# Kernel optimization log

Measured on AMD Instinct MI355X. Metric: run time of the kernel, lower is better.

## Reference

```python
import jax, jax.numpy as jnp
import numpy as np

N, E = 10000, 80000
D, D_EDGE, L = 32, 16, 3
D2 = D * D


def layer_norm(x, g, b, eps=1e-5):
    m = jnp.mean(x, axis=-1, keepdims=True)
    v = jnp.var(x, axis=-1, keepdims=True)
    return (x - m) / jnp.sqrt(v + eps) * g + b


def setup_inputs() -> dict:
    key = jax.random.key(0)
    ks = jax.random.split(key, 16)
    s_e = 1.0 / np.sqrt(D_EDGE)
    s_d = 1.0 / np.sqrt(D)
    s_f = 1.0 / np.sqrt(L * D)
    return {
        "x": jax.random.normal(ks[0], (N, D), dtype=jnp.float32),
        "edge_index": jax.random.randint(ks[1], (2, E), 0, N),
        "edge_attr": jax.random.normal(ks[2], (E, D_EDGE), dtype=jnp.float32),
        # shared edge MLP: Linear(d_edge_in -> d^2) + LayerNorm(d^2) + ReLU
        "emlp_w": jax.random.uniform(ks[3], (D2, D_EDGE), jnp.float32, -s_e, s_e),
        "emlp_b": jnp.zeros((D2,), jnp.float32),
        "emlp_ln_g": jnp.ones((D2,), jnp.float32),
        "emlp_ln_b": jnp.zeros((D2,), jnp.float32),
        # per-layer params (stacked over L layers)
        "root_w": jax.random.uniform(ks[4], (L, D, D), jnp.float32, -s_d, s_d),  # NNConv root lin (no bias)
        "conv_b": jnp.zeros((L, D), jnp.float32),                                # NNConv bias
        "res_w": jax.random.uniform(ks[5], (L, D, D), jnp.float32, -s_d, s_d),
        "res_b": jnp.zeros((L, D), jnp.float32),
        "ln_g": jnp.ones((L, D), jnp.float32),
        "ln_b": jnp.zeros((L, D), jnp.float32),
        # fusion: Linear(L*d -> d) + LayerNorm(d) + ReLU
        "fuse_w": jax.random.uniform(ks[6], (D, L * D), jnp.float32, -s_f, s_f),
        "fuse_b": jnp.zeros((D,), jnp.float32),
        "fuse_ln_g": jnp.ones((D,), jnp.float32),
        "fuse_ln_b": jnp.zeros((D,), jnp.float32),
    }


def reference(x, edge_index, edge_attr, emlp_w, emlp_b, emlp_ln_g, emlp_ln_b,
              root_w, conv_b, res_w, res_b, ln_g, ln_b,
              fuse_w, fuse_b, fuse_ln_g, fuse_ln_b):
    n_nodes = x.shape[0]
    src, tgt = edge_index[0], edge_index[1]
    # Shared edge MLP applied to the same edge_attr in every layer -> identical
    # per-edge weight matrices; compute once. [E, d_in, d_out]
    h = layer_norm(edge_attr @ emlp_w.T + emlp_b, emlp_ln_g, emlp_ln_b)
    We = jax.nn.relu(h).reshape(-1, D, D)
    x_src_gatherer = src
    outputs = []
    for l in range(L):
        x_res = x @ res_w[l].T + res_b[l]
        # NNConv message: x_j @ W_e, scatter-add to target nodes
        msg = jnp.einsum('ed,edf->ef', x[x_src_gatherer], We)  # [E, d]
        agg = jax.ops.segment_sum(msg, tgt, num_segments=n_nodes)
        h = agg + x @ root_w[l].T + conv_b[l]
        # dropout is identity in eval mode
        x = layer_norm(h + x_res, ln_g[l], ln_b[l])
        outputs.append(x)
    fused = jnp.concatenate(outputs, axis=-1) @ fuse_w.T + fuse_b
    fused = jax.nn.relu(layer_norm(fused, fuse_ln_g, fuse_ln_b))
    return fused
```

## Files before the change

kernel.cpp:

```cpp
#include <hip/hip_runtime.h>

#define NN 10000
#define EE 80000
#define DD 32
#define DEDGE 16
#define LL 3
#define D2V 1024
#define NTILE 2500

typedef __attribute__((ext_vector_type(8))) short short8v;
typedef __attribute__((ext_vector_type(16))) float f32x16;

__device__ __forceinline__ unsigned short bf16rne(float x) {
    unsigned u = __float_as_uint(x);
    return (unsigned short)((u + 0x7FFF + ((u >> 16) & 1)) >> 16);
}
__device__ __forceinline__ float bf16tof(unsigned short h) {
    return __uint_as_float(((unsigned)h) << 16);
}
__device__ __forceinline__ uint4 pack8(const unsigned short* u) {
    uint4 r;
    r.x = (unsigned)u[0] | ((unsigned)u[1] << 16);
    r.y = (unsigned)u[2] | ((unsigned)u[3] << 16);
    r.z = (unsigned)u[4] | ((unsigned)u[5] << 16);
    r.w = (unsigned)u[6] | ((unsigned)u[7] << 16);
    return r;
}

__global__ __launch_bounds__(256) void setup1_kernel(
    const int* __restrict__ ei,
    const float* __restrict__ w, const float* __restrict__ wb,
    const float* __restrict__ lg, const float* __restrict__ lb,
    int* __restrict__ cnt, float* __restrict__ st,
    uint4* __restrict__ afh, uint4* __restrict__ afl, uint4* __restrict__ a2f) {
    const int bid = blockIdx.x;
    const int t = threadIdx.x;
    if (bid < 313) {
        const int e = bid * 256 + t;
        if (e < EE) atomicAdd(&cnt[ei[EE + e]], 1);
    } else if (bid < 377) {
        const int r0 = (bid - 313) * 16;
        const int k = t >> 4, j = t & 15;
        float acc = 0.f;
#pragma unroll
        for (int r = 0; r < 16; ++r)
            acc = fmaf(w[(r0 + r) * DEDGE + k], w[(r0 + r) * DEDGE + j], acc);
        atomicAdd(&st[t], acc * (1.f / D2V));
        if (t < DEDGE) {
            float s = 0.f, q = 0.f;
#pragma unroll
            for (int r = 0; r < 16; ++r) {
                s += w[(r0 + r) * DEDGE + t];
                q = fmaf(wb[r0 + r], w[(r0 + r) * DEDGE + t], q);
            }
            atomicAdd(&st[256 + t], s * (1.f / D2V));
            atomicAdd(&st[272 + t], q * (1.f / D2V));
        } else if (t == 16) {
            float s = 0.f, s2 = 0.f;
#pragma unroll
            for (int r = 0; r < 16; ++r) {
                s += wb[r0 + r];
                s2 = fmaf(wb[r0 + r], wb[r0 + r], s2);
            }
            atomicAdd(&st[288], s * (1.f / D2V));
            atomicAdd(&st[289], s2 * (1.f / D2V));
        }
    } else {
        const int tid = (bid - 377) * 256 + t;
        if (tid >= 32 * 64) return;
        const int d = tid >> 6, l = tid & 63;
        const int row = l & 31, kh = l >> 5;
        const int r = d * 32 + row;
        const float g = lg[r];
        unsigned short uh[8], ul[8];
#pragma unroll
        for (int i = 0; i < 8; ++i) {
            const float v = g * w[r * DEDGE + kh * 8 + i];
            const unsigned short h = bf16rne(v);
            uh[i] = h;
            ul[i] = bf16rne(v - bf16tof(h));
        }
        afh[d * 64 + l] = pack8(uh);
        afl[d * 64 + l] = pack8(ul);
        if (kh == 0) {
            const float bg = g * wb[r];
            const float lbv = lb[r];
            const unsigned short bgh = bf16rne(bg);
            const unsigned short bgl = bf16rne(bg - bf16tof(bgh));
            const unsigned short gh = bf16rne(g);
            const unsigned short gl = bf16rne(g - bf16tof(gh));
            const unsigned short lbh = bf16rne(lbv);
            const unsigned short lbl = bf16rne(lbv - bf16tof(lbh));
            unsigned short sarr[8] = {bgh, bgl, bgh, gh, gl, gh, lbh, lbl};
            a2f[d * 64 + l] = pack8(sarr);
        } else {
            a2f[d * 64 + l] = make_uint4(0, 0, 0, 0);
        }
    }
}

__global__ __launch_bounds__(1024) void scan_kernel(int* __restrict__ cur, int* __restrict__ off) {
    __shared__ int s[1024];
    const int t = threadIdx.x;
    const int base = t * 10;
    int loc[10];
    int run = 0;
#pragma unroll
    for (int i = 0; i < 10; ++i) {
        const int idx = base + i;
        const int v = (idx < NN) ? cur[idx] : 0;
        loc[i] = run;
        run += v;
    }
    s[t] = run;
    __syncthreads();
    for (int o = 1; o < 1024; o <<= 1) {
        const int v = (t >= o) ? s[t - o] : 0;
        __syncthreads();
        s[t] += v;
        __syncthreads();
    }
    const int excl = s[t] - run;
#pragma unroll
    for (int i = 0; i < 10; ++i) {
        const int idx = base + i;
        if (idx < NN) {
            off[idx] = excl + loc[i];
            cur[idx] = excl + loc[i];
        }
    }
    if (t == 1023) off[NN] = s[1023];
}

__global__ __launch_bounds__(256) void stats_edge_perm2(const float* __restrict__ eattr,
                                                        const float* __restrict__ st,
                                                        const int* __restrict__ ei,
                                                        int* __restrict__ cur,
                                                        uint4* __restrict__ bfh,
                                                        uint4* __restrict__ bfl,
                                                        uint4* __restrict__ b2f,
                                                        int* __restrict__ sperm) {
    const int e = blockIdx.x * 256 + threadIdx.x;
    if (e >= EE) return;
    const int tgt = ei[EE + e];
    const int p = atomicAdd(&cur[tgt], 1);
    sperm[p] = ei[e];
    float ea[16];
    {
        const float4* ep = (const float4*)(eattr + e * DEDGE);
#pragma unroll
        for (int c = 0; c < 4; ++c) {
            const float4 t4 = ep[c];
            ea[4 * c] = t4.x; ea[4 * c + 1] = t4.y; ea[4 * c + 2] = t4.z; ea[4 * c + 3] = t4.w;
        }
    }
    float m = st[288];
#pragma unroll
    for (int k = 0; k < 16; ++k) m = fmaf(st[256 + k], ea[k], m);
    float ex2 = st[289];
#pragma unroll
    for (int k = 0; k < 16; ++k) {
        float tv = 2.f * st[272 + k];
#pragma unroll
        for (int j = 0; j < 16; ++j) tv = fmaf(st[k * 16 + j], ea[j], tv);
        ex2 = fmaf(tv, ea[k], ex2);
    }
    const float var = fmaxf(ex2 - m * m, 0.f);
    const float inv = rsqrtf(var + 1e-5f);
    const float nmi = -m * inv;
    const int tt = p >> 5, col = p & 31;
#pragma unroll
    for (int h = 0; h < 2; ++h) {
        unsigned short uh[8], ul[8];
#pragma unroll
        for (int i = 0; i < 8; ++i) {
            const float v = inv * ea[8 * h + i];
            const unsigned short a = bf16rne(v);
            uh[i] = a;
            ul[i] = bf16rne(v - bf16tof(a));
        }
        bfh[tt * 64 + h * 32 + col] = pack8(uh);
        bfl[tt * 64 + h * 32 + col] = pack8(ul);
    }
    const unsigned short ivh = bf16rne(inv);
    const unsigned short ivl = bf16rne(inv - bf16tof(ivh));
    const unsigned short nmh = bf16rne(nmi);
    const unsigned short nml = bf16rne(nmi - bf16tof(nmh));
    const unsigned short one = 0x3F80;
    unsigned short s[8] = {ivh, ivh, ivl, nmh, nmh, nml, one, one};
    b2f[tt * 64 + col] = pack8(s);
    b2f[tt * 64 + 32 + col] = make_uint4(0, 0, 0, 0);
}

__global__ __launch_bounds__(512) void edge_mfma_lds(
    const float* __restrict__ x, const int* __restrict__ sperm,
    const uint4* __restrict__ afh, const uint4* __restrict__ afl, const uint4* __restrict__ a2f,
    const uint4* __restrict__ bfh, const uint4* __restrict__ bfl, const uint4* __restrict__ b2f,
    float* __restrict__ msgout) {
    __shared__ uint4 lafh[2048];
    __shared__ uint4 lafl[2048];
    __shared__ uint4 la2c[1024];
    const int t = threadIdx.x;
    for (int i = t; i < 2048; i += 512) {
        lafh[i] = afh[i];
        lafl[i] = afl[i];
    }
    for (int i = t; i < 1024; i += 512)
        la2c[i] = a2f[(i >> 5) * 64 + (i & 31)];
    __syncthreads();

    const int lane = t & 63;
    const int w = blockIdx.x * 8 + (t >> 6);
    if (w >= NTILE) return;
    const int col = lane & 31, hi = lane >> 5;
    const int p = w * 32 + col;
    const int si = sperm[p];
    float xr[32];
    {
        const float4* xp = (const float4*)(x + si * DD);
#pragma unroll
        for (int c = 0; c < 8; ++c) {
            const float4 t4 = xp[c];
            xr[4 * c] = t4.x; xr[4 * c + 1] = t4.y; xr[4 * c + 2] = t4.z; xr[4 * c + 3] = t4.w;
        }
    }
    const short8v bh = ((const short8v*)bfh)[w * 64 + lane];
    const short8v bl = ((const short8v*)bfl)[w * 64 + lane];
    const short8v b2 = ((const short8v*)b2f)[w * 64 + lane];
    float mg[16];
#pragma unroll
    for (int i = 0; i < 16; ++i) mg[i] = 0.f;
#pragma unroll
    for (int d = 0; d < 32; ++d) {
        const short8v ah = ((const short8v*)lafh)[d * 64 + lane];
        const short8v al = ((const short8v*)lafl)[d * 64 + lane];
        const short8v a2 = ((const short8v*)la2c)[d * 32 + col];
        f32x16 C;
#pragma unroll
        for (int r = 0; r < 16; ++r) C[r] = 0.f;
        C = __builtin_amdgcn_mfma_f32_32x32x16_bf16(ah, bh, C, 0, 0, 0);
        C = __builtin_amdgcn_mfma_f32_32x32x16_bf16(ah, bl, C, 0, 0, 0);
        C = __builtin_amdgcn_mfma_f32_32x32x16_bf16(al, bh, C, 0, 0, 0);
        C = __builtin_amdgcn_mfma_f32_32x32x16_bf16(a2, b2, C, 0, 0, 0);
        const float xd = xr[d];
#pragma unroll
        for (int r = 0; r < 16; ++r) mg[r] = fmaf(xd, fmaxf(C[r], 0.f), mg[r]);
    }
    float* op = msgout + p * DD + hi * 4;
#pragma unroll
    for (int q = 0; q < 4; ++q)
        *(float4*)(op + q * 8) = make_float4(mg[4 * q], mg[4 * q + 1], mg[4 * q + 2], mg[4 * q + 3]);
}

__global__ __launch_bounds__(256) void node_wave_kernel(
    const float* __restrict__ x, const float* __restrict__ msg,
    const int* __restrict__ off,
    const float* __restrict__ root_w, const float* __restrict__ conv_b,
    const float* __restrict__ res_w, const float* __restrict__ res_b,
    const float* __restrict__ lng, const float* __restrict__ lnb,
    float* __restrict__ out) {
    const int lane = threadIdx.x & 63;
    const int w = (blockIdx.x * 256 + threadIdx.x) >> 6;
    const int hi = lane >> 5, f = lane & 31;
    const int n = w * 2 + hi;
    float wrow[32];
    {
        const float4* rp = (const float4*)(root_w + f * DD);
        const float4* sp = (const float4*)(res_w + f * DD);
#pragma unroll
        for (int c = 0; c < 8; ++c) {
            const float4 a = rp[c];
            const float4 b = sp[c];
            wrow[4 * c] = a.x + b.x; wrow[4 * c + 1] = a.y + b.y;
            wrow[4 * c + 2] = a.z + b.z; wrow[4 * c + 3] = a.w + b.w;
        }
    }
    float acc = conv_b[f] + res_b[f];
    const int k0 = off[n], k1 = off[n + 1];
    for (int k = k0; k < k1; ++k) acc += msg[k * DD + f];
    const float xl = x[n * DD + f];
#pragma unroll
    for (int d = 0; d < DD; ++d) acc = fmaf(__shfl(xl, hi * 32 + d), wrow[d], acc);
    float s1 = acc, s2 = acc * acc;
#pragma unroll
    for (int o = 16; o >= 1; o >>= 1) {
        s1 += __shfl_xor(s1, o);
        s2 += __shfl_xor(s2, o);
    }
    const float m = s1 * (1.f / 32.f);
    const float v = s2 * (1.f / 32.f) - m * m;
    const float inv = rsqrtf(v + 1e-5f);
    out[n * DD + f] = fmaf((acc - m) * inv, lng[f], lnb[f]);
}

__global__ __launch_bounds__(256) void node_fuse_kernel(
    const float* __restrict__ x, const float* __restrict__ msg,
    const int* __restrict__ off,
    const float* __restrict__ root_w, const float* __restrict__ conv_b,
    const float* __restrict__ res_w, const float* __restrict__ res_b,
    const float* __restrict__ lng, const float* __restrict__ lnb,
    const float* __restrict__ o0, const float* __restrict__ o1,
    const float* __restrict__ fw, const float* __restrict__ fb,
    const float* __restrict__ fg, const float* __restrict__ fbb,
    float* __restrict__ out) {
    const int lane = threadIdx.x & 63;
    const int w = (blockIdx.x * 256 + threadIdx.x) >> 6;
    const int hi = lane >> 5, f = lane & 31;
    const int n = w * 2 + hi;
    float o2v;
    {
        float wrow[32];
        {
            const float4* rp = (const float4*)(root_w + f * DD);
            const float4* sp = (const float4*)(res_w + f * DD);
#pragma unroll
            for (int c = 0; c < 8; ++c) {
                const float4 a = rp[c];
                const float4 b = sp[c];
                wrow[4 * c] = a.x + b.x; wrow[4 * c + 1] = a.y + b.y;
                wrow[4 * c + 2] = a.z + b.z; wrow[4 * c + 3] = a.w + b.w;
            }
        }
        float acc = conv_b[f] + res_b[f];
        const int k0 = off[n], k1 = off[n + 1];
        for (int k = k0; k < k1; ++k) acc += msg[k * DD + f];
        const float xl = x[n * DD + f];
#pragma unroll
        for (int d = 0; d < DD; ++d) acc = fmaf(__shfl(xl, hi * 32 + d), wrow[d], acc);
        float s1 = acc, s2 = acc * acc;
#pragma unroll
        for (int o = 16; o >= 1; o >>= 1) {
            s1 += __shfl_xor(s1, o);
            s2 += __shfl_xor(s2, o);
        }
        const float m = s1 * (1.f / 32.f);
        const float v = s2 * (1.f / 32.f) - m * m;
        const float inv = rsqrtf(v + 1e-5f);
        o2v = fmaf((acc - m) * inv, lng[f], lnb[f]);
    }
    float fr[96];
    {
        const float4* fp = (const float4*)(fw + f * 96);
#pragma unroll
        for (int c = 0; c < 24; ++c) {
            const float4 t4 = fp[c];
            fr[4 * c] = t4.x; fr[4 * c + 1] = t4.y; fr[4 * c + 2] = t4.z; fr[4 * c + 3] = t4.w;
        }
    }
    float acc = fb[f];
    const float c0 = o0[n * DD + f], c1 = o1[n * DD + f];
#pragma unroll
    for (int d = 0; d < DD; ++d) acc = fmaf(__shfl(c0, hi * 32 + d), fr[d], acc);
#pragma unroll
    for (int d = 0; d < DD; ++d) acc = fmaf(__shfl(c1, hi * 32 + d), fr[32 + d], acc);
#pragma unroll
    for (int d = 0; d < DD; ++d) acc = fmaf(__shfl(o2v, hi * 32 + d), fr[64 + d], acc);
    float s1 = acc, s2 = acc * acc;
#pragma unroll
    for (int o = 16; o >= 1; o >>= 1) {
        s1 += __shfl_xor(s1, o);
        s2 += __shfl_xor(s2, o);
    }
    const float m = s1 * (1.f / 32.f);
    const float v = s2 * (1.f / 32.f) - m * m;
    const float inv = rsqrtf(v + 1e-5f);
    out[n * DD + f] = fmaxf(fmaf((acc - m) * inv, fg[f], fbb[f]), 0.f);
}

extern "C" void kernel_launch(void* const* d_in, const int* in_sizes, int n_in,
                              void* d_out, int out_size, void* d_ws, size_t ws_size,
                              hipStream_t stream) {
    const float* x   = (const float*)d_in[0];
    const int*   ei  = (const int*)d_in[1];
    const float* ea  = (const float*)d_in[2];
    const float* emw = (const float*)d_in[3];
    const float* emb = (const float*)d_in[4];
    const float* elg = (const float*)d_in[5];
    const float* elb = (const float*)d_in[6];
    const float* rootw = (const float*)d_in[7];
    const float* convb = (const float*)d_in[8];
    const float* resw  = (const float*)d_in[9];
    const float* resb  = (const float*)d_in[10];
    const float* lng   = (const float*)d_in[11];
    const float* lnb   = (const float*)d_in[12];
    const float* fw    = (const float*)d_in[13];
    const float* fb    = (const float*)d_in[14];
    const float* flg   = (const float*)d_in[15];
    const float* flb   = (const float*)d_in[16];
    float* doutp = (float*)d_out;

    const size_t U4N = 2048 * 3 + (size_t)NTILE * 64 * 3;
    const size_t FR0 = U4N * 4;
    const size_t FTOT = FR0 + (size_t)EE * DD + 2 * (size_t)NN * DD + 320;
    const size_t ITOT = 2 * (NN + 1) + 2 * (size_t)EE;
    const size_t PRIMARY_NEED = FTOT * 4 + ITOT * 4 + 256;

    if (ws_size < PRIMARY_NEED) return;

    uint4* u4 = (uint4*)d_ws;
    uint4* afh = u4;
    uint4* afl = afh + 2048;
    uint4* a2f = afl + 2048;
    uint4* bfh = a2f + 2048;
    uint4* bfl = bfh + (size_t)NTILE * 64;
    uint4* b2f = bfl + (size_t)NTILE * 64;
    float* wsf = (float*)d_ws;
    float* msg  = wsf + FR0;
    float* out0 = msg + (size_t)EE * DD;
    float* out1 = out0 + NN * DD;
    float* st   = out1 + NN * DD;
    int* cur   = (int*)(st + 320);
    int* off   = cur + (NN + 1);
    int* spare = off + (NN + 1);
    int* sperm = spare + EE;
    (void)spare;

    hipMemsetAsync(st, 0, (320 + NN + 1) * sizeof(float), stream);
    setup1_kernel<<<385, 256, 0, stream>>>(ei, emw, emb, elg, elb, cur, st, afh, afl, a2f);
    scan_kernel<<<1, 1024, 0, stream>>>(cur, off);
    stats_edge_perm2<<<313, 256, 0, stream>>>(ea, st, ei, cur, bfh, bfl, b2f, sperm);

    edge_mfma_lds<<<313, 512, 0, stream>>>(x, sperm, afh, afl, a2f, bfh, bfl, b2f, msg);
    node_wave_kernel<<<1250, 256, 0, stream>>>(x, msg, off,
        rootw, convb, resw, resb, lng, lnb, out0);
    edge_mfma_lds<<<313, 512, 0, stream>>>(out0, sperm, afh, afl, a2f, bfh, bfl, b2f, msg);
    node_wave_kernel<<<1250, 256, 0, stream>>>(out0, msg, off,
        rootw + D2V, convb + DD, resw + D2V, resb + DD, lng + DD, lnb + DD, out1);
    edge_mfma_lds<<<313, 512, 0, stream>>>(out1, sperm, afh, afl, a2f, bfh, bfl, b2f, msg);
    node_fuse_kernel<<<1250, 256, 0, stream>>>(out1, msg, off,
        rootw + 2 * D2V, convb + 2 * DD, resw + 2 * D2V, resb + 2 * DD,
        lng + 2 * DD, lnb + 2 * DD,
        out0, out1, fw, fb, flg, flb, doutp);
}
```

Baseline: 169.8 us.

## Merge setup, scan and edge-permutation kernels into one grid-synchronized kernel

Replaces the setup kernel, the single-block scan kernel and the edge permutation/stats kernel with one persistent 385-block kernel that uses global atomic counters and spin-waits as grid barriers. Zeroing of the counters and stats now happens inside the kernel, so the large memset shrinks to a 4-int reset. The aim is to remove three launch gaps and the memset. In exchange it relies on all 385 blocks being co-resident, and the scan now runs in a single 256-thread block while the other blocks spin.

Result: slower. 304.5 us (+79.3%).

```diff
diff --git a/kernel.cpp b/kernel.cpp
--- a/kernel.cpp
+++ b/kernel.cpp
@@ -27,31 +27,52 @@
     return r;
 }
 
-__global__ __launch_bounds__(256) void setup1_kernel(
-    const int* __restrict__ ei,
-    const float* __restrict__ w, const float* __restrict__ wb,
-    const float* __restrict__ lg, const float* __restrict__ lb,
-    int* __restrict__ cnt, float* __restrict__ st,
-    uint4* __restrict__ afh, uint4* __restrict__ afl, uint4* __restrict__ a2f) {
+__device__ __forceinline__ void block_spin(int* p, int target) {
+    if (threadIdx.x == 0) {
+        while (atomicAdd(p, 0) < target) __builtin_amdgcn_s_sleep(16);
+    }
+    __syncthreads();
+    __threadfence();
+}
+
+__global__ __launch_bounds__(256) void merged_csr(
+    const int* __restrict__ ei, const float* __restrict__ eattr,
+    const float* __restrict__ emw, const float* __restrict__ emb,
+    const float* __restrict__ elg, const float* __restrict__ elb,
+    int* __restrict__ syncc, int* __restrict__ cur, int* __restrict__ off,
+    float* __restrict__ st,
+    uint4* __restrict__ afh, uint4* __restrict__ afl, uint4* __restrict__ a2f,
+    uint4* __restrict__ bfh, uint4* __restrict__ bfl, uint4* __restrict__ b2f,
+    int* __restrict__ sperm)
+{
+    __shared__ int sscan[256];
     const int bid = blockIdx.x;
     const int t = threadIdx.x;
+    const int g = bid * 256 + t;
+
+    if (g <= NN) cur[g] = 0;
+    if (g < 320) st[g] = 0.f;
+    __threadfence();
+    __syncthreads();
+    if (t == 0) atomicAdd(&syncc[0], 1);
+    block_spin(&syncc[0], 385);
+
     if (bid < 313) {
-        const int e = bid * 256 + t;
-        if (e < EE) atomicAdd(&cnt[ei[EE + e]], 1);
+        if (g < EE) atomicAdd(&cur[ei[EE + g]], 1);
     } else if (bid < 377) {
         const int r0 = (bid - 313) * 16;
         const int k = t >> 4, j = t & 15;
         float acc = 0.f;
 #pragma unroll
         for (int r = 0; r < 16; ++r)
-            acc = fmaf(w[(r0 + r) * DEDGE + k], w[(r0 + r) * DEDGE + j], acc);
+            acc = fmaf(emw[(r0 + r) * DEDGE + k], emw[(r0 + r) * DEDGE + j], acc);
         atomicAdd(&st[t], acc * (1.f / D2V));
         if (t < DEDGE) {
             float s = 0.f, q = 0.f;
 #pragma unroll
             for (int r = 0; r < 16; ++r) {
-                s += w[(r0 + r) * DEDGE + t];
-                q = fmaf(wb[r0 + r], w[(r0 + r) * DEDGE + t], q);
+                s += emw[(r0 + r) * DEDGE + t];
+                q = fmaf(emb[r0 + r], emw[(r0 + r) * DEDGE + t], q);
             }
             atomicAdd(&st[256 + t], s * (1.f / D2V));
             atomicAdd(&st[272 + t], q * (1.f / D2V));
@@ -59,23 +80,22 @@
             float s = 0.f, s2 = 0.f;
 #pragma unroll
             for (int r = 0; r < 16; ++r) {
-                s += wb[r0 + r];
-                s2 = fmaf(wb[r0 + r], wb[r0 + r], s2);
+                s += emb[r0 + r];
+                s2 = fmaf(emb[r0 + r], emb[r0 + r], s2);
             }
             atomicAdd(&st[288], s * (1.f / D2V));
             atomicAdd(&st[289], s2 * (1.f / D2V));
         }
     } else {
-        const int tid = (bid - 377) * 256 + t;
-        if (tid >= 32 * 64) return;
-        const int d = tid >> 6, l = tid & 63;
+        const int tid2 = (bid - 377) * 256 + t;
+        const int d = tid2 >> 6, l = tid2 & 63;
         const int row = l & 31, kh = l >> 5;
         const int r = d * 32 + row;
-        const float g = lg[r];
+        const float gg = elg[r];
         unsigned short uh[8], ul[8];
 #pragma unroll
         for (int i = 0; i < 8; ++i) {
-            const float v = g * w[r * DEDGE + kh * 8 + i];
+            const float v = gg * emw[r * DEDGE + kh * 8 + i];
             const unsigned short h = bf16rne(v);
             uh[i] = h;
             ul[i] = bf16rne(v - bf16tof(h));
@@ -83,12 +103,12 @@
         afh[d * 64 + l] = pack8(uh);
         afl[d * 64 + l] = pack8(ul);
         if (kh == 0) {
-            const float bg = g * wb[r];
-            const float lbv = lb[r];
+            const float bg = gg * emb[r];
+            const float lbv = elb[r];
             const unsigned short bgh = bf16rne(bg);
             const unsigned short bgl = bf16rne(bg - bf16tof(bgh));
-            const unsigned short gh = bf16rne(g);
-            const unsigned short gl = bf16rne(g - bf16tof(gh));
+            const unsigned short gh = bf16rne(gg);
+            const unsigned short gl = bf16rne(gg - bf16tof(gh));
             const unsigned short lbh = bf16rne(lbv);
             const unsigned short lbl = bf16rne(lbv - bf16tof(lbh));
             unsigned short sarr[8] = {bgh, bgl, bgh, gh, gl, gh, lbh, lbl};
@@ -97,99 +117,98 @@
             a2f[d * 64 + l] = make_uint4(0, 0, 0, 0);
         }
     }
-}
-
-__global__ __launch_bounds__(1024) void scan_kernel(int* __restrict__ cur, int* __restrict__ off) {
-    __shared__ int s[1024];
-    const int t = threadIdx.x;
-    const int base = t * 10;
-    int loc[10];
-    int run = 0;
-#pragma unroll
-    for (int i = 0; i < 10; ++i) {
-        const int idx = base + i;
-        const int v = (idx < NN) ? cur[idx] : 0;
-        loc[i] = run;
-        run += v;
-    }
-    s[t] = run;
+    __threadfence();
     __syncthreads();
-    for (int o = 1; o < 1024; o <<= 1) {
-        const int v = (t >= o) ? s[t - o] : 0;
+    if (t == 0) atomicAdd(&syncc[1], 1);
+
+    if (bid == 0) {
+        block_spin(&syncc[1], 385);
+        const int per = (NN + 255) / 256;
+        const int base = t * per;
+        int sum = 0;
+        for (int i = 0; i < per; ++i) {
+            const int idx = base + i;
+            if (idx < NN) sum += cur[idx];
+        }
+        sscan[t] = sum;
         __syncthreads();
-        s[t] += v;
+        for (int o = 1; o < 256; o <<= 1) {
+            const int v = (t >= o) ? sscan[t - o] : 0;
+            __syncthreads();
+            sscan[t] += v;
+            __syncthreads();
+        }
+        int run = sscan[t] - sum;
+        for (int i = 0; i < per; ++i) {
+            const int idx = base + i;
+            if (idx < NN) {
+                const int v = cur[idx];
+                off[idx] = run;
+                cur[idx] = run;
+                run += v;
+            }
+        }
+        if (t == 255) off[NN] = run;
+        __threadfence();
         __syncthreads();
-    }
-    const int excl = s[t] - run;
-#pragma unroll
-    for (int i = 0; i < 10; ++i) {
-        const int idx = base + i;
-        if (idx < NN) {
-            off[idx] = excl + loc[i];
-            cur[idx] = excl + loc[i];
-        }
-    }
-    if (t == 1023) off[NN] = s[1023];
-}
-
-__global__ __launch_bounds__(256) void stats_edge_perm2(const float* __restrict__ eattr,
-                                                        const float* __restrict__ st,
-                                                        const int* __restrict__ ei,
-                                                        int* __restrict__ cur,
-                                                        uint4* __restrict__ bfh,
-                                                        uint4* __restrict__ bfl,
-                                                        uint4* __restrict__ b2f,
-                                                        int* __restrict__ sperm) {
-    const int e = blockIdx.x * 256 + threadIdx.x;
-    if (e >= EE) return;
-    const int tgt = ei[EE + e];
-    const int p = atomicAdd(&cur[tgt], 1);
-    sperm[p] = ei[e];
-    float ea[16];
-    {
-        const float4* ep = (const float4*)(eattr + e * DEDGE);
-#pragma unroll
-        for (int c = 0; c < 4; ++c) {
-            const float4 t4 = ep[c];
-            ea[4 * c] = t4.x; ea[4 * c + 1] = t4.y; ea[4 * c + 2] = t4.z; ea[4 * c + 3] = t4.w;
-        }
-    }
-    float m = st[288];
-#pragma unroll
-    for (int k = 0; k < 16; ++k) m = fmaf(st[256 + k], ea[k], m);
-    float ex2 = st[289];
-#pragma unroll
-    for (int k = 0; k < 16; ++k) {
-        float tv = 2.f * st[272 + k];
-#pragma unroll
-        for (int j = 0; j < 16; ++j) tv = fmaf(st[k * 16 + j], ea[j], tv);
-        ex2 = fmaf(tv, ea[k], ex2);
-    }
-    const float var = fmaxf(ex2 - m * m, 0.f);
-    const float inv = rsqrtf(var + 1e-5f);
-    const float nmi = -m * inv;
-    const int tt = p >> 5, col = p & 31;
-#pragma unroll
-    for (int h = 0; h < 2; ++h) {
-        unsigned short uh[8], ul[8];
-#pragma unroll
-        for (int i = 0; i < 8; ++i) {
-            const float v = inv * ea[8 * h + i];
-            const unsigned short a = bf16rne(v);
-            uh[i] = a;
-            ul[i] = bf16rne(v - bf16tof(a));
-        }
-        bfh[tt * 64 + h * 32 + col] = pack8(uh);
-        bfl[tt * 64 + h * 32 + col] = pack8(ul);
-    }
-    const unsigned short ivh = bf16rne(inv);
-    const unsigned short ivl = bf16rne(inv - bf16tof(ivh));
-    const unsigned short nmh = bf16rne(nmi);
-    const unsigned short nml = bf16rne(nmi - bf16tof(nmh));
-    const unsigned short one = 0x3F80;
-    unsigned short s[8] = {ivh, ivh, ivl, nmh, nmh, nml, one, one};
-    b2f[tt * 64 + col] = pack8(s);
-    b2f[tt * 64 + 32 + col] = make_uint4(0, 0, 0, 0);
+        if (t == 0) atomicAdd(&syncc[2], 1);
+    }
+
+    if (bid < 313) {
+        block_spin(&syncc[2], 1);
+        if (g < EE) {
+            const int e = g;
+            const int tgt = ei[EE + e];
+            const int p = atomicAdd(&cur[tgt], 1);
+            sperm[p] = ei[e];
+            float ea[16];
+            {
+                const float4* ep = (const float4*)(eattr + e * DEDGE);
+#pragma unroll
+                for (int c = 0; c < 4; ++c) {
+                    const float4 t4 = ep[c];
+                    ea[4 * c] = t4.x; ea[4 * c + 1] = t4.y;
+                    ea[4 * c + 2] = t4.z; ea[4 * c + 3] = t4.w;
+                }
+            }
+            float m = st[288];
+#pragma unroll
+            for (int k = 0; k < 16; ++k) m = fmaf(st[256 + k], ea[k], m);
+            float ex2 = st[289];
+#pragma unroll
+            for (int k = 0; k < 16; ++k) {
+                float tv = 2.f * st[272 + k];
+#pragma unroll
+                for (int j = 0; j < 16; ++j) tv = fmaf(st[k * 16 + j], ea[j], tv);
+                ex2 = fmaf(tv, ea[k], ex2);
+            }
+            const float var = fmaxf(ex2 - m * m, 0.f);
+            const float inv = rsqrtf(var + 1e-5f);
+            const float nmi = -m * inv;
+            const int tt = p >> 5, col = p & 31;
+#pragma unroll
+            for (int h = 0; h < 2; ++h) {
+                unsigned short uh[8], ul[8];
+#pragma unroll
+                for (int i = 0; i < 8; ++i) {
+                    const float v = inv * ea[8 * h + i];
+                    const unsigned short a = bf16rne(v);
+                    uh[i] = a;
+                    ul[i] = bf16rne(v - bf16tof(a));
+                }
+                bfh[tt * 64 + h * 32 + col] = pack8(uh);
+                bfl[tt * 64 + h * 32 + col] = pack8(ul);
+            }
+            const unsigned short ivh = bf16rne(inv);
+            const unsigned short ivl = bf16rne(inv - bf16tof(ivh));
+            const unsigned short nmh = bf16rne(nmi);
+            const unsigned short nml = bf16rne(nmi - bf16tof(nmh));
+            const unsigned short one = 0x3F80;
+            unsigned short s[8] = {ivh, ivh, ivl, nmh, nmh, nml, one, one};
+            b2f[tt * 64 + col] = pack8(s);
+            b2f[tt * 64 + 32 + col] = make_uint4(0, 0, 0, 0);
+        }
+    }
 }
 
 __global__ __launch_bounds__(512) void edge_mfma_lds(
@@ -392,7 +411,7 @@
     const size_t U4N = 2048 * 3 + (size_t)NTILE * 64 * 3;
     const size_t FR0 = U4N * 4;
     const size_t FTOT = FR0 + (size_t)EE * DD + 2 * (size_t)NN * DD + 320;
-    const size_t ITOT = 2 * (NN + 1) + 2 * (size_t)EE;
+    const size_t ITOT = 2 * (NN + 1) + 2 * (size_t)EE + 8;
     const size_t PRIMARY_NEED = FTOT * 4 + ITOT * 4 + 256;
 
     if (ws_size < PRIMARY_NEED) return;
@@ -413,12 +432,13 @@
     int* off   = cur + (NN + 1);
     int* spare = off + (NN + 1);
     int* sperm = spare + EE;
+    int* syncc = sperm + EE;
     (void)spare;
 
-    hipMemsetAsync(st, 0, (320 + NN + 1) * sizeof(float), stream);
-    setup1_kernel<<<385, 256, 0, stream>>>(ei, emw, emb, elg, elb, cur, st, afh, afl, a2f);
-    scan_kernel<<<1, 1024, 0, stream>>>(cur, off);
-    stats_edge_perm2<<<313, 256, 0, stream>>>(ea, st, ei, cur, bfh, bfl, b2f, sperm);
+    hipMemsetAsync(syncc, 0, 4 * sizeof(int), stream);
+    merged_csr<<<385, 256, 0, stream>>>(ei, ea, emw, emb, elg, elb,
+                                        syncc, cur, off, st,
+                                        afh, afl, a2f, bfh, bfl, b2f, sperm);
 
     edge_mfma_lds<<<313, 512, 0, stream>>>(x, sperm, afh, afl, a2f, bfh, bfl, b2f, msg);
     node_wave_kernel<<<1250, 256, 0, stream>>>(x, msg, off,
```
